# Kernel tuning notes

Measured on AMD Instinct MI355X. Metric: run time of the kernel, lower is better.

Reference implementation:

```python
import jax, jax.numpy as jnp
import numpy as np

EMB = 768
HEADS = 12
HD = EMB // HEADS
FF = 4 * EMB
EPS = 1e-5


def gelu_tanh(x):
    c = jnp.sqrt(jnp.asarray(2.0 / jnp.pi, x.dtype))
    return 0.5 * x * (1.0 + jnp.tanh(c * (x + 0.044715 * x ** 3)))


def layernorm(x, scale, shift):
    mean = x.mean(-1, keepdims=True)
    var = ((x - mean) ** 2).mean(-1, keepdims=True)
    return scale * (x - mean) / jnp.sqrt(var + EPS) + shift


def setup_inputs() -> dict:
    key = jax.random.key(0)
    ks = jax.random.split(key, 12)
    s = 0.02
    return {
        "x": jax.random.normal(ks[0], (8, 1024, EMB), jnp.float32),
        "Wq": jax.random.normal(ks[1], (EMB, EMB), jnp.float32) * s,
        "Wk": jax.random.normal(ks[2], (EMB, EMB), jnp.float32) * s,
        "Wv": jax.random.normal(ks[3], (EMB, EMB), jnp.float32) * s,
        "Wo": jax.random.normal(ks[4], (EMB, EMB), jnp.float32) * s,
        "bo": jnp.zeros((EMB,), jnp.float32),
        "W1": jax.random.normal(ks[5], (EMB, FF), jnp.float32) * s,
        "b1": jnp.zeros((FF,), jnp.float32),
        "W2": jax.random.normal(ks[6], (FF, EMB), jnp.float32) * s,
        "b2": jnp.zeros((EMB,), jnp.float32),
        "ln1_scale": jnp.ones((EMB,), jnp.float32),
        "ln1_shift": jnp.zeros((EMB,), jnp.float32),
        "ln2_scale": jnp.ones((EMB,), jnp.float32),
        "ln2_shift": jnp.zeros((EMB,), jnp.float32),
    }


def reference(x, Wq, Wk, Wv, Wo, bo, W1, b1, W2, b2,
              ln1_scale, ln1_shift, ln2_scale, ln2_shift):
    B, T, _ = x.shape
    inp = x
    h = layernorm(x, ln1_scale, ln1_shift)
    # QKV projections (no bias, qkv_bias=False)
    q = (h @ Wq).reshape(B, T, HEADS, HD).transpose(0, 2, 1, 3)  # [B,H,T,hd]
    k = (h @ Wk).reshape(B, T, HEADS, HD).transpose(0, 2, 1, 3)
    v = (h @ Wv).reshape(B, T, HEADS, HD).transpose(0, 2, 1, 3)
    scores = jnp.einsum('bhqd,bhkd->bhqk', q, k)
    causal = jnp.triu(jnp.ones((T, T), bool), k=1)
    scores = jnp.where(causal, -jnp.inf, scores)
    attn = jax.nn.softmax(scores / jnp.sqrt(jnp.asarray(HD, x.dtype)), axis=-1)
    ctx = jnp.einsum('bhqk,bhkd->bhqd', attn, v)
    ctx = ctx.transpose(0, 2, 1, 3).reshape(B, T, EMB)
    attn_out = ctx @ Wo + bo
    x = inp + attn_out  # dropout is identity (rate 0 / eval)
    inp = x
    h = layernorm(x, ln2_scale, ln2_shift)
    ff = gelu_tanh(h @ W1 + b1) @ W2 + b2
    return inp + ff
```

## Files before the change

### kernel.cpp

```cpp
#include <hip/hip_runtime.h>
#include <hip/hip_bf16.h>
#include <stdint.h>
#include <stddef.h>

#define EMB 768
#define FFD 3072
#define NHEAD 12
#define HD 64
#define SEQ 1024
#define NTOK 8192
#define QKVW 2304

typedef unsigned short u16;
typedef __attribute__((ext_vector_type(8))) short short8;
typedef __attribute__((ext_vector_type(4))) float f32x4;

__device__ __forceinline__ u16 f2bf(float f) {
  union { float f; uint32_t u; } w; w.f = f;
  uint32_t x = w.u + 0x7fffu + ((w.u >> 16) & 1u);
  return (u16)(x >> 16);
}

__device__ __forceinline__ uint32_t pkbf(float lo, float hi) {
  __hip_bfloat162 h = __float22bfloat162_rn(float2{lo, hi});
  union { __hip_bfloat162 h; uint32_t u; } cv; cv.h = h;
  return cv.u;
}

__device__ __forceinline__ void g2l16(const void* g, void* l) {
  __builtin_amdgcn_global_load_lds(
      (const __attribute__((address_space(1))) void*)g,
      (__attribute__((address_space(3))) void*)l, 16, 0, 0);
}

__global__ __launch_bounds__(256)
void transpose_kernel(const float* __restrict__ in, u16* __restrict__ out, int K, int N) {
  __shared__ float tile[32][33];
  const int n0 = blockIdx.x * 32, k0 = blockIdx.y * 32;
  const int tx = threadIdx.x & 31;
  const int ty = threadIdx.x >> 5;
#pragma unroll
  for (int i = 0; i < 32; i += 8)
    tile[ty + i][tx] = in[(size_t)(k0 + ty + i) * N + n0 + tx];
  __syncthreads();
#pragma unroll
  for (int i = 0; i < 32; i += 8)
    out[(size_t)(n0 + ty + i) * K + k0 + tx] = f2bf(tile[tx][ty + i]);
}

__global__ __launch_bounds__(256)
void transpose_qkv_kernel(const float* __restrict__ Wq, const float* __restrict__ Wk,
                          const float* __restrict__ Wv, u16* __restrict__ out) {
  __shared__ float tile[32][33];
  const float* in = blockIdx.z == 0 ? Wq : (blockIdx.z == 1 ? Wk : Wv);
  u16* o = out + (size_t)blockIdx.z * EMB * EMB;
  const int n0 = blockIdx.x * 32, k0 = blockIdx.y * 32;
  const int tx = threadIdx.x & 31;
  const int ty = threadIdx.x >> 5;
#pragma unroll
  for (int i = 0; i < 32; i += 8)
    tile[ty + i][tx] = in[(size_t)(k0 + ty + i) * EMB + n0 + tx];
  __syncthreads();
#pragma unroll
  for (int i = 0; i < 32; i += 8)
    o[(size_t)(n0 + ty + i) * EMB + k0 + tx] = f2bf(tile[tx][ty + i]);
}

__global__ __launch_bounds__(256)
void ln_kernel(const float* __restrict__ x, const float* __restrict__ sc,
               const float* __restrict__ sh, u16* __restrict__ out) {
  const int row = blockIdx.x;
  const int tid = threadIdx.x;
  const float* xr = x + (size_t)row * EMB;
  float v0 = xr[tid], v1 = xr[tid + 256], v2 = xr[tid + 512];
  float s = v0 + v1 + v2;
  float ss = v0 * v0 + v1 * v1 + v2 * v2;
#pragma unroll
  for (int m = 1; m < 64; m <<= 1) { s += __shfl_xor(s, m, 64); ss += __shfl_xor(ss, m, 64); }
  __shared__ float red[8];
  const int wave = tid >> 6, lane = tid & 63;
  if (lane == 0) { red[wave] = s; red[wave + 4] = ss; }
  __syncthreads();
  s = red[0] + red[1] + red[2] + red[3];
  ss = red[4] + red[5] + red[6] + red[7];
  const float mean = s * (1.f / EMB);
  const float var = ss * (1.f / EMB) - mean * mean;
  const float inv = rsqrtf(var + 1e-5f);
  u16* orow = out + (size_t)row * EMB;
  orow[tid]       = f2bf((v0 - mean) * inv * sc[tid]       + sh[tid]);
  orow[tid + 256] = f2bf((v1 - mean) * inv * sc[tid + 256] + sh[tid + 256]);
  orow[tid + 512] = f2bf((v2 - mean) * inv * sc[tid + 512] + sh[tid + 512]);
}

template <int EPI, int MT, bool SWAP>
__global__ __launch_bounds__(256)
void gemm_kernel(const u16* __restrict__ A, const u16* __restrict__ BT,
                 void* __restrict__ Cp, const float* __restrict__ bias,
                 const float* __restrict__ res, u16* __restrict__ vTp,
                 int M, int N, int K) {
  constexpr int MI = MT / 32;
  __shared__ u16 As[MT * 64];
  __shared__ u16 Bs[128 * 64];

  const int nwg = gridDim.x * gridDim.y;
  const int orig = blockIdx.y * gridDim.x + blockIdx.x;
  const int swz = (orig & 7) * (nwg >> 3) + (orig >> 3);
  const int m0 = (swz / gridDim.x) * MT;
  const int n0 = (swz % gridDim.x) * 128;

  const int tid = threadIdx.x;
  const int wave = tid >> 6, lane = tid & 63;
  const int wr = wave >> 1, wc = wave & 1;
  const int r = lane & 15, g = lane >> 4;
  const int lrow = lane >> 3;
  const int lelem = (lane & 7) * 8;

  f32x4 acc[MI][4] = {};

  const int nkt = K >> 6;
  for (int kt = 0; kt < nkt; ++kt) {
    const int k0 = kt << 6;
    if (kt) __syncthreads();
#pragma unroll
    for (int q = 0; q < MT / 32; ++q) {
      const int chunk = q * 4 + wave;
      const int row = chunk * 8 + lrow;
      const int e = lelem ^ ((row & 7) << 3);
      g2l16(A + (size_t)(m0 + row) * K + k0 + e, As + chunk * 512);
    }
#pragma unroll
    for (int q = 0; q < 4; ++q) {
      const int chunk = q * 4 + wave;
      const int row = chunk * 8 + lrow;
      const int e = lelem ^ ((row & 7) << 3);
      g2l16(BT + (size_t)(n0 + row) * K + k0 + e, Bs + chunk * 512);
    }
    __syncthreads();
#pragma unroll
    for (int kk = 0; kk < 2; ++kk) {
      short8 af[MI], bf[4];
#pragma unroll
      for (int mi = 0; mi < MI; ++mi) {
        const int row = wr * (MT / 2) + mi * 16 + r;
        af[mi] = *(const short8*)(As + row * 64 + ((kk * 32 + g * 8) ^ ((row & 7) << 3)));
      }
#pragma unroll
      for (int ni = 0; ni < 4; ++ni) {
        const int row = wc * 64 + ni * 16 + r;
        bf[ni] = *(const short8*)(Bs + row * 64 + ((kk * 32 + g * 8) ^ ((row & 7) << 3)));
      }
#pragma unroll
      for (int mi = 0; mi < MI; ++mi)
#pragma unroll
        for (int ni = 0; ni < 4; ++ni) {
          if constexpr (SWAP)
            acc[mi][ni] = __builtin_amdgcn_mfma_f32_16x16x32_bf16(bf[ni], af[mi], acc[mi][ni], 0, 0, 0);
          else
            acc[mi][ni] = __builtin_amdgcn_mfma_f32_16x16x32_bf16(af[mi], bf[ni], acc[mi][ni], 0, 0, 0);
        }
    }
  }

  if constexpr (SWAP) {
#pragma unroll
    for (int mi = 0; mi < MI; ++mi) {
      const int m = m0 + wr * (MT / 2) + mi * 16 + r;
#pragma unroll
      for (int ni = 0; ni < 4; ++ni) {
        const int nb = n0 + wc * 64 + ni * 16 + 4 * g;
        if constexpr (EPI == 1) {
          const float4 bs = *(const float4*)(bias + nb);
          const float4 rs = *(const float4*)(res + (size_t)m * N + nb);
          float4 o;
          o.x = acc[mi][ni][0] + bs.x + rs.x;
          o.y = acc[mi][ni][1] + bs.y + rs.y;
          o.z = acc[mi][ni][2] + bs.z + rs.z;
          o.w = acc[mi][ni][3] + bs.w + rs.w;
          *(float4*)((float*)Cp + (size_t)m * N + nb) = o;
        } else {
          const float4 bs = *(const float4*)(bias + nb);
          float tj[4];
#pragma unroll
          for (int j = 0; j < 4; ++j) {
            float t = acc[mi][ni][j] + (&bs.x)[j];
            float e = __expf(1.5957691216057308f * (t + 0.044715f * t * t * t));
            tj[j] = 0.5f * t * (1.f + (1.f - 2.f / (e + 1.f)));
          }
          uint2 w2;
          w2.x = pkbf(tj[0], tj[1]);
          w2.y = pkbf(tj[2], tj[3]);
          *(uint2*)((u16*)Cp + (size_t)m * N + nb) = w2;
        }
      }
    }
  } else {
#pragma unroll
    for (int mi = 0; mi < MI; ++mi)
#pragma unroll
      for (int ni = 0; ni < 4; ++ni) {
        const int rowb = m0 + wr * (MT / 2) + mi * 16 + 4 * g;
        const int col = n0 + wc * 64 + ni * 16 + r;
        u16 pk[4];
#pragma unroll
        for (int j = 0; j < 4; ++j) pk[j] = f2bf(acc[mi][ni][j]);
        if (col < 1536) {
#pragma unroll
          for (int j = 0; j < 4; ++j)
            ((u16*)Cp)[(size_t)(rowb + j) * N + col] = pk[j];
        } else {
          uint2 w2;
          w2.x = (uint32_t)pk[0] | ((uint32_t)pk[1] << 16);
          w2.y = (uint32_t)pk[2] | ((uint32_t)pk[3] << 16);
          *(uint2*)(vTp + (size_t)(col - 1536) * NTOK + rowb) = w2;
        }
      }
  }
}

#define CEXP 0.18033688011112042f

__global__ __launch_bounds__(256, 3)
void attn_kernel(const u16* __restrict__ qkv, const u16* __restrict__ vT,
                 u16* __restrict__ ctx) {
  const int bh = blockIdx.x;
  const int qt = blockIdx.y;
  const int b = bh / NHEAD, h = bh % NHEAD;
  const int tid = threadIdx.x;
  const int wave = tid >> 6, lane = tid & 63;
  const int r = lane & 15, g = lane >> 4;

  __shared__ u16 Kb[2][64 * 64];
  __shared__ u16 Vb[2][64 * 64];
  __shared__ u16 Pt[4][16 * 64];

  const int qw = qt * 128 + wave * 32;
  const int tok0 = b * SEQ;

  short8 aq[2][2];
#pragma unroll
  for (int qf = 0; qf < 2; ++qf) {
    const u16* qb = qkv + (size_t)(tok0 + qw + qf * 16 + r) * QKVW + h * HD;
    aq[qf][0] = *(const short8*)(qb + g * 8);
    aq[qf][1] = *(const short8*)(qb + 32 + g * 8);
  }

  float l_st[2] = {0.f, 0.f};
  f32x4 oc[2][4] = {};

  const int sr = tid >> 3;
  const int sc = (tid & 7) * 8;
  const int nt = 2 * qt + 2;

  const u16* kg = qkv + (size_t)tok0 * QKVW + EMB + h * HD;
  const u16* vg = vT + (size_t)(h * HD) * NTOK + tok0;
  const int e0 = sc ^ ((sr & 7) << 3);

  auto stage = [&](int buf, int kt) {
    const size_t koff = (size_t)kt * 64;
    u16* kb = (u16*)Kb[buf] + wave * 512;
    u16* vb = (u16*)Vb[buf] + wave * 512;
    g2l16(kg + (koff + sr) * QKVW + e0, kb);
    g2l16(kg + (koff + sr + 32) * QKVW + e0, kb + 2048);
    g2l16(vg + (size_t)sr * NTOK + koff + e0, vb);
    g2l16(vg + (size_t)(sr + 32) * NTOK + koff + e0, vb + 2048);
  };

  stage(0, 0);
  for (int kb = 0; kb < nt; ++kb) {
    __syncthreads();
    const int cur = kb & 1;
    if (kb + 1 < nt) stage(cur ^ 1, kb + 1);

    const int kv0 = kb * 64;
    if (kv0 > qw + 31) continue;

    short8 kf[4][2];
#pragma unroll
    for (int nf = 0; nf < 4; ++nf) {
      const int row = nf * 16 + r;
#pragma unroll
      for (int kk = 0; kk < 2; ++kk)
        kf[nf][kk] = *(const short8*)((char*)Kb[cur] + row * 128 +
                                      ((kk * 64 + g * 16) ^ ((row & 7) << 4)));
    }
    short8 bv[2][4];
#pragma unroll
    for (int half = 0; half < 2; ++half)
#pragma unroll
      for (int nd = 0; nd < 4; ++nd) {
        const int vr = nd * 16 + r;
        bv[half][nd] = *(const short8*)((char*)Vb[cur] + vr * 128 +
                       ((half * 64 + g * 16) ^ ((vr & 7) << 4)));
      }

#pragma unroll
    for (int qf = 0; qf < 2; ++qf) {
      f32x4 st[4];
#pragma unroll
      for (int nf = 0; nf < 4; ++nf) {
        f32x4 z = {};
        z = __builtin_amdgcn_mfma_f32_16x16x32_bf16(kf[nf][0], aq[qf][0], z, 0, 0, 0);
        z = __builtin_amdgcn_mfma_f32_16x16x32_bf16(kf[nf][1], aq[qf][1], z, 0, 0, 0);
        st[nf] = z;
      }
      if (kv0 + 63 > qw + qf * 16) {
        const int qg = qw + qf * 16 + r;
#pragma unroll
        for (int nf = 0; nf < 4; ++nf)
#pragma unroll
          for (int j = 0; j < 4; ++j)
            if (kv0 + nf * 16 + 4 * g + j > qg) st[nf][j] = -3e38f;
      }
      float p[4][4];
      float ps = 0.f;
#pragma unroll
      for (int nf = 0; nf < 4; ++nf)
#pragma unroll
        for (int j = 0; j < 4; ++j) {
          const float pe = exp2f(st[nf][j] * CEXP);
          p[nf][j] = pe;
          ps += pe;
        }
      ps += __shfl_xor(ps, 16);
      ps += __shfl_xor(ps, 32);
      l_st[qf] += ps;

      u16* Pw = (u16*)Pt[wave];
#pragma unroll
      for (int nf = 0; nf < 4; ++nf) {
        uint2 w2;
        w2.x = pkbf(p[nf][0], p[nf][1]);
        w2.y = pkbf(p[nf][2], p[nf][3]);
        *(uint2*)((char*)Pw + r * 128 + ((nf * 32 + g * 8) ^ ((r & 7) << 4))) = w2;
      }
#pragma unroll
      for (int half = 0; half < 2; ++half) {
        short8 pa = *(const short8*)((char*)Pw + r * 128 +
                                     ((half * 64 + g * 16) ^ ((r & 7) << 4)));
#pragma unroll
        for (int nd = 0; nd < 4; ++nd)
          oc[qf][nd] = __builtin_amdgcn_mfma_f32_16x16x32_bf16(pa, bv[half][nd], oc[qf][nd], 0, 0, 0);
      }
    }
  }

#pragma unroll
  for (int qf = 0; qf < 2; ++qf) {
    const float rl = 1.f / l_st[qf];
#pragma unroll
    for (int j = 0; j < 4; ++j) {
      const float rj = __shfl(rl, 4 * g + j, 16);
      const size_t row = (size_t)tok0 + qw + qf * 16 + 4 * g + j;
#pragma unroll
      for (int nd = 0; nd < 4; ++nd)
        ctx[row * EMB + h * HD + nd * 16 + r] = f2bf(oc[qf][nd][j] * rj);
    }
  }
}

extern "C" void kernel_launch(void* const* d_in, const int* in_sizes, int n_in,
                              void* d_out, int out_size, void* d_ws, size_t ws_size,
                              hipStream_t stream) {
  const float* x    = (const float*)d_in[0];
  const float* Wq   = (const float*)d_in[1];
  const float* Wk   = (const float*)d_in[2];
  const float* Wv   = (const float*)d_in[3];
  const float* Wo   = (const float*)d_in[4];
  const float* bo   = (const float*)d_in[5];
  const float* W1   = (const float*)d_in[6];
  const float* b1   = (const float*)d_in[7];
  const float* W2   = (const float*)d_in[8];
  const float* b2   = (const float*)d_in[9];
  const float* ln1s = (const float*)d_in[10];
  const float* ln1b = (const float*)d_in[11];
  const float* ln2s = (const float*)d_in[12];
  const float* ln2b = (const float*)d_in[13];

  char* p = (char*)d_ws;
  u16* qkvT = (u16*)p; p += (size_t)QKVW * EMB * 2;
  u16* woT  = (u16*)p; p += (size_t)EMB * EMB * 2;
  u16* w1T  = (u16*)p; p += (size_t)FFD * EMB * 2;
  u16* w2T  = (u16*)p; p += (size_t)EMB * FFD * 2;
  u16* h1   = (u16*)p; p += (size_t)NTOK * EMB * 2;
  u16* qkv  = (u16*)p; p += (size_t)NTOK * QKVW * 2;
  float* x2 = (float*)p; p += (size_t)NTOK * EMB * 4;
  u16* ff1  = (u16*)p; p += (size_t)NTOK * FFD * 2;
  u16* ctxb = h1;
  u16* h2   = qkv;
  u16* vT   = ff1;

  if (ws_size < (size_t)(p - (char*)d_ws)) return;

  dim3 blk(256);
  transpose_qkv_kernel<<<dim3(24, 24, 3), blk, 0, stream>>>(Wq, Wk, Wv, qkvT);
  transpose_kernel<<<dim3(24, 24), blk, 0, stream>>>(Wo, woT, EMB, EMB);
  transpose_kernel<<<dim3(96, 24), blk, 0, stream>>>(W1, w1T, EMB, FFD);
  transpose_kernel<<<dim3(24, 96), blk, 0, stream>>>(W2, w2T, FFD, EMB);

  ln_kernel<<<NTOK, blk, 0, stream>>>(x, ln1s, ln1b, h1);
  gemm_kernel<3, 128, false><<<dim3(18, 64), blk, 0, stream>>>(h1, qkvT, qkv, nullptr, nullptr, vT, NTOK, QKVW, EMB);
  attn_kernel<<<dim3(96, 8), blk, 0, stream>>>(qkv, vT, ctxb);
  gemm_kernel<1, 64, true><<<dim3(6, 128), blk, 0, stream>>>(ctxb, woT, x2, bo, x, nullptr, NTOK, EMB, EMB);
  ln_kernel<<<NTOK, blk, 0, stream>>>(x2, ln2s, ln2b, h2);
  gemm_kernel<2, 128, true><<<dim3(24, 64), blk, 0, stream>>>(h2, w1T, ff1, b1, nullptr, nullptr, NTOK, FFD, EMB);
  gemm_kernel<1, 64, true><<<dim3(6, 128), blk, 0, stream>>>(ff1, w2T, (float*)d_out, b2, x2, nullptr, NTOK, EMB, FFD);
}
```

Before: 233.6 us.

## Store residual in bf16, split QKV kernel with vectorized Q/K stores

Adds a dedicated QKV GEMM kernel that picks the MFMA operand order per tile, so the Q/K outputs use packed 64-bit row stores into a compact 1536-wide buffer instead of scattered 16-bit stores. V is still written transposed. The attention residual x2 is now stored in bf16 instead of fp32, with a new bf16 layernorm kernel and a bf16-residual epilogue in the final GEMM. This cuts write and read traffic, but rounding the residual stream to bf16 lowers accuracy.

```diff
diff --git a/kernel.cpp b/kernel.cpp
--- a/kernel.cpp
+++ b/kernel.cpp
@@ -10,6 +10,7 @@
 #define SEQ 1024
 #define NTOK 8192
 #define QKVW 2304
+#define QKW 1536
 
 typedef unsigned short u16;
 typedef __attribute__((ext_vector_type(8))) short short8;
@@ -19,6 +20,10 @@
   union { float f; uint32_t u; } w; w.f = f;
   uint32_t x = w.u + 0x7fffu + ((w.u >> 16) & 1u);
   return (u16)(x >> 16);
+}
+
+__device__ __forceinline__ float bf2f(uint32_t v) {
+  union { uint32_t u; float f; } c; c.u = v << 16; return c.f;
 }
 
 __device__ __forceinline__ uint32_t pkbf(float lo, float hi) {
@@ -92,11 +97,37 @@
   orow[tid + 512] = f2bf((v2 - mean) * inv * sc[tid + 512] + sh[tid + 512]);
 }
 
+__global__ __launch_bounds__(256)
+void ln_bf_kernel(const u16* __restrict__ x, const float* __restrict__ sc,
+                  const float* __restrict__ sh, u16* __restrict__ out) {
+  const int row = blockIdx.x;
+  const int tid = threadIdx.x;
+  const u16* xr = x + (size_t)row * EMB;
+  float v0 = bf2f(xr[tid]), v1 = bf2f(xr[tid + 256]), v2 = bf2f(xr[tid + 512]);
+  float s = v0 + v1 + v2;
+  float ss = v0 * v0 + v1 * v1 + v2 * v2;
+#pragma unroll
+  for (int m = 1; m < 64; m <<= 1) { s += __shfl_xor(s, m, 64); ss += __shfl_xor(ss, m, 64); }
+  __shared__ float red[8];
+  const int wave = tid >> 6, lane = tid & 63;
+  if (lane == 0) { red[wave] = s; red[wave + 4] = ss; }
+  __syncthreads();
+  s = red[0] + red[1] + red[2] + red[3];
+  ss = red[4] + red[5] + red[6] + red[7];
+  const float mean = s * (1.f / EMB);
+  const float var = ss * (1.f / EMB) - mean * mean;
+  const float inv = rsqrtf(var + 1e-5f);
+  u16* orow = out + (size_t)row * EMB;
+  orow[tid]       = f2bf((v0 - mean) * inv * sc[tid]       + sh[tid]);
+  orow[tid + 256] = f2bf((v1 - mean) * inv * sc[tid + 256] + sh[tid + 256]);
+  orow[tid + 512] = f2bf((v2 - mean) * inv * sc[tid + 512] + sh[tid + 512]);
+}
+
 template <int EPI, int MT, bool SWAP>
 __global__ __launch_bounds__(256)
 void gemm_kernel(const u16* __restrict__ A, const u16* __restrict__ BT,
                  void* __restrict__ Cp, const float* __restrict__ bias,
-                 const float* __restrict__ res, u16* __restrict__ vTp,
+                 const float* __restrict__ res, const u16* __restrict__ res16,
                  int M, int N, int K) {
   constexpr int MI = MT / 32;
   __shared__ u16 As[MT * 64];
@@ -161,36 +192,137 @@
     }
   }
 
-  if constexpr (SWAP) {
+#pragma unroll
+  for (int mi = 0; mi < MI; ++mi) {
+    const int m = m0 + wr * (MT / 2) + mi * 16 + r;
+#pragma unroll
+    for (int ni = 0; ni < 4; ++ni) {
+      const int nb = n0 + wc * 64 + ni * 16 + 4 * g;
+      if constexpr (EPI == 1) {
+        const float4 bs = *(const float4*)(bias + nb);
+        const float4 rs = *(const float4*)(res + (size_t)m * N + nb);
+        float4 o;
+        o.x = acc[mi][ni][0] + bs.x + rs.x;
+        o.y = acc[mi][ni][1] + bs.y + rs.y;
+        o.z = acc[mi][ni][2] + bs.z + rs.z;
+        o.w = acc[mi][ni][3] + bs.w + rs.w;
+        *(float4*)((float*)Cp + (size_t)m * N + nb) = o;
+      } else if constexpr (EPI == 2) {
+        const float4 bs = *(const float4*)(bias + nb);
+        float tj[4];
+#pragma unroll
+        for (int j = 0; j < 4; ++j) {
+          float t = acc[mi][ni][j] + (&bs.x)[j];
+          float e = __expf(1.5957691216057308f * (t + 0.044715f * t * t * t));
+          tj[j] = 0.5f * t * (1.f + (1.f - 2.f / (e + 1.f)));
+        }
+        uint2 w2;
+        w2.x = pkbf(tj[0], tj[1]);
+        w2.y = pkbf(tj[2], tj[3]);
+        *(uint2*)((u16*)Cp + (size_t)m * N + nb) = w2;
+      } else if constexpr (EPI == 4) {
+        const float4 bs = *(const float4*)(bias + nb);
+        const float4 rs = *(const float4*)(res + (size_t)m * N + nb);
+        uint2 w2;
+        w2.x = pkbf(acc[mi][ni][0] + bs.x + rs.x, acc[mi][ni][1] + bs.y + rs.y);
+        w2.y = pkbf(acc[mi][ni][2] + bs.z + rs.z, acc[mi][ni][3] + bs.w + rs.w);
+        *(uint2*)((u16*)Cp + (size_t)m * N + nb) = w2;
+      } else {
+        const float4 bs = *(const float4*)(bias + nb);
+        const uint2 r2 = *(const uint2*)(res16 + (size_t)m * N + nb);
+        float4 o;
+        o.x = acc[mi][ni][0] + bs.x + bf2f(r2.x & 0xffffu);
+        o.y = acc[mi][ni][1] + bs.y + bf2f(r2.x >> 16);
+        o.z = acc[mi][ni][2] + bs.z + bf2f(r2.y & 0xffffu);
+        o.w = acc[mi][ni][3] + bs.w + bf2f(r2.y >> 16);
+        *(float4*)((float*)Cp + (size_t)m * N + nb) = o;
+      }
+    }
+  }
+}
+
+__global__ __launch_bounds__(256)
+void qkv_kernel(const u16* __restrict__ A, const u16* __restrict__ BT,
+                u16* __restrict__ qkp, u16* __restrict__ vTp) {
+  constexpr int MT = 128, MI = 4, K = EMB, N = QKVW;
+  __shared__ u16 As[MT * 64];
+  __shared__ u16 Bs[128 * 64];
+
+  const int nwg = gridDim.x * gridDim.y;
+  const int orig = blockIdx.y * gridDim.x + blockIdx.x;
+  const int swz = (orig & 7) * (nwg >> 3) + (orig >> 3);
+  const int m0 = (swz / gridDim.x) * MT;
+  const int n0 = (swz % gridDim.x) * 128;
+
+  const int tid = threadIdx.x;
+  const int wave = tid >> 6, lane = tid & 63;
+  const int wr = wave >> 1, wc = wave & 1;
+  const int r = lane & 15, g = lane >> 4;
+  const int lrow = lane >> 3;
+  const int lelem = (lane & 7) * 8;
+
+  f32x4 acc[MI][4] = {};
+  const bool isQK = (n0 < 1536);
+
+  const int nkt = K >> 6;
+  for (int kt = 0; kt < nkt; ++kt) {
+    const int k0 = kt << 6;
+    if (kt) __syncthreads();
+#pragma unroll
+    for (int q = 0; q < MT / 32; ++q) {
+      const int chunk = q * 4 + wave;
+      const int row = chunk * 8 + lrow;
+      const int e = lelem ^ ((row & 7) << 3);
+      g2l16(A + (size_t)(m0 + row) * K + k0 + e, As + chunk * 512);
+    }
+#pragma unroll
+    for (int q = 0; q < 4; ++q) {
+      const int chunk = q * 4 + wave;
+      const int row = chunk * 8 + lrow;
+      const int e = lelem ^ ((row & 7) << 3);
+      g2l16(BT + (size_t)(n0 + row) * K + k0 + e, Bs + chunk * 512);
+    }
+    __syncthreads();
+#pragma unroll
+    for (int kk = 0; kk < 2; ++kk) {
+      short8 af[MI], bf[4];
+#pragma unroll
+      for (int mi = 0; mi < MI; ++mi) {
+        const int row = wr * (MT / 2) + mi * 16 + r;
+        af[mi] = *(const short8*)(As + row * 64 + ((kk * 32 + g * 8) ^ ((row & 7) << 3)));
+      }
+#pragma unroll
+      for (int ni = 0; ni < 4; ++ni) {
+        const int row = wc * 64 + ni * 16 + r;
+        bf[ni] = *(const short8*)(Bs + row * 64 + ((kk * 32 + g * 8) ^ ((row & 7) << 3)));
+      }
+      if (isQK) {
+#pragma unroll
+        for (int mi = 0; mi < MI; ++mi)
+#pragma unroll
+          for (int ni = 0; ni < 4; ++ni)
+            acc[mi][ni] = __builtin_amdgcn_mfma_f32_16x16x32_bf16(bf[ni], af[mi], acc[mi][ni], 0, 0, 0);
+      } else {
+#pragma unroll
+        for (int mi = 0; mi < MI; ++mi)
+#pragma unroll
+          for (int ni = 0; ni < 4; ++ni)
+            acc[mi][ni] = __builtin_amdgcn_mfma_f32_16x16x32_bf16(af[mi], bf[ni], acc[mi][ni], 0, 0, 0);
+      }
+    }
+  }
+
+  if (isQK) {
 #pragma unroll
     for (int mi = 0; mi < MI; ++mi) {
       const int m = m0 + wr * (MT / 2) + mi * 16 + r;
 #pragma unroll
       for (int ni = 0; ni < 4; ++ni) {
         const int nb = n0 + wc * 64 + ni * 16 + 4 * g;
-        if constexpr (EPI == 1) {
-          const float4 bs = *(const float4*)(bias + nb);
-          const float4 rs = *(const float4*)(res + (size_t)m * N + nb);
-          float4 o;
-          o.x = acc[mi][ni][0] + bs.x + rs.x;
-          o.y = acc[mi][ni][1] + bs.y + rs.y;
-          o.z = acc[mi][ni][2] + bs.z + rs.z;
-          o.w = acc[mi][ni][3] + bs.w + rs.w;
-          *(float4*)((float*)Cp + (size_t)m * N + nb) = o;
-        } else {
-          const float4 bs = *(const float4*)(bias + nb);
-          float tj[4];
-#pragma unroll
-          for (int j = 0; j < 4; ++j) {
-            float t = acc[mi][ni][j] + (&bs.x)[j];
-            float e = __expf(1.5957691216057308f * (t + 0.044715f * t * t * t));
-            tj[j] = 0.5f * t * (1.f + (1.f - 2.f / (e + 1.f)));
-          }
-          uint2 w2;
-          w2.x = pkbf(tj[0], tj[1]);
-          w2.y = pkbf(tj[2], tj[3]);
-          *(uint2*)((u16*)Cp + (size_t)m * N + nb) = w2;
-        }
+        uint2 w2;
+        w2.x = pkbf(acc[mi][ni][0], acc[mi][ni][1]);
+        w2.y = pkbf(acc[mi][ni][2], acc[mi][ni][3]);
+        *(uint2*)(qkp + (size_t)m * QKW + nb) = w2;
       }
     }
   } else {
@@ -200,19 +332,10 @@
       for (int ni = 0; ni < 4; ++ni) {
         const int rowb = m0 + wr * (MT / 2) + mi * 16 + 4 * g;
         const int col = n0 + wc * 64 + ni * 16 + r;
-        u16 pk[4];
-#pragma unroll
-        for (int j = 0; j < 4; ++j) pk[j] = f2bf(acc[mi][ni][j]);
-        if (col < 1536) {
-#pragma unroll
-          for (int j = 0; j < 4; ++j)
-            ((u16*)Cp)[(size_t)(rowb + j) * N + col] = pk[j];
-        } else {
-          uint2 w2;
-          w2.x = (uint32_t)pk[0] | ((uint32_t)pk[1] << 16);
-          w2.y = (uint32_t)pk[2] | ((uint32_t)pk[3] << 16);
-          *(uint2*)(vTp + (size_t)(col - 1536) * NTOK + rowb) = w2;
-        }
+        uint2 w2;
+        w2.x = pkbf(acc[mi][ni][0], acc[mi][ni][1]);
+        w2.y = pkbf(acc[mi][ni][2], acc[mi][ni][3]);
+        *(uint2*)(vTp + (size_t)(col - 1536) * NTOK + rowb) = w2;
       }
   }
 }
@@ -220,7 +343,7 @@
 #define CEXP 0.18033688011112042f
 
 __global__ __launch_bounds__(256, 3)
-void attn_kernel(const u16* __restrict__ qkv, const u16* __restrict__ vT,
+void attn_kernel(const u16* __restrict__ qk, const u16* __restrict__ vT,
                  u16* __restrict__ ctx) {
   const int bh = blockIdx.x;
   const int qt = blockIdx.y;
@@ -239,7 +362,7 @@
   short8 aq[2][2];
 #pragma unroll
   for (int qf = 0; qf < 2; ++qf) {
-    const u16* qb = qkv + (size_t)(tok0 + qw + qf * 16 + r) * QKVW + h * HD;
+    const u16* qb = qk + (size_t)(tok0 + qw + qf * 16 + r) * QKW + h * HD;
     aq[qf][0] = *(const short8*)(qb + g * 8);
     aq[qf][1] = *(const short8*)(qb + 32 + g * 8);
   }
@@ -251,7 +374,7 @@
   const int sc = (tid & 7) * 8;
   const int nt = 2 * qt + 2;
 
-  const u16* kg = qkv + (size_t)tok0 * QKVW + EMB + h * HD;
+  const u16* kg = qk + (size_t)tok0 * QKW + EMB + h * HD;
   const u16* vg = vT + (size_t)(h * HD) * NTOK + tok0;
   const int e0 = sc ^ ((sr & 7) << 3);
 
@@ -259,8 +382,8 @@
     const size_t koff = (size_t)kt * 64;
     u16* kb = (u16*)Kb[buf] + wave * 512;
     u16* vb = (u16*)Vb[buf] + wave * 512;
-    g2l16(kg + (koff + sr) * QKVW + e0, kb);
-    g2l16(kg + (koff + sr + 32) * QKVW + e0, kb + 2048);
+    g2l16(kg + (koff + sr) * QKW + e0, kb);
+    g2l16(kg + (koff + sr + 32) * QKW + e0, kb + 2048);
     g2l16(vg + (size_t)sr * NTOK + koff + e0, vb);
     g2l16(vg + (size_t)(sr + 32) * NTOK + koff + e0, vb + 2048);
   };
@@ -382,11 +505,11 @@
   u16* w1T  = (u16*)p; p += (size_t)FFD * EMB * 2;
   u16* w2T  = (u16*)p; p += (size_t)EMB * FFD * 2;
   u16* h1   = (u16*)p; p += (size_t)NTOK * EMB * 2;
-  u16* qkv  = (u16*)p; p += (size_t)NTOK * QKVW * 2;
-  float* x2 = (float*)p; p += (size_t)NTOK * EMB * 4;
+  u16* qk   = (u16*)p; p += (size_t)NTOK * QKW * 2;
+  u16* x2bf = (u16*)p; p += (size_t)NTOK * EMB * 2;
   u16* ff1  = (u16*)p; p += (size_t)NTOK * FFD * 2;
   u16* ctxb = h1;
-  u16* h2   = qkv;
+  u16* h2   = qk;
   u16* vT   = ff1;
 
   if (ws_size < (size_t)(p - (char*)d_ws)) return;
@@ -398,10 +521,10 @@
   transpose_kernel<<<dim3(24, 96), blk, 0, stream>>>(W2, w2T, FFD, EMB);
 
   ln_kernel<<<NTOK, blk, 0, stream>>>(x, ln1s, ln1b, h1);
-  gemm_kernel<3, 128, false><<<dim3(18, 64), blk, 0, stream>>>(h1, qkvT, qkv, nullptr, nullptr, vT, NTOK, QKVW, EMB);
-  attn_kernel<<<dim3(96, 8), blk, 0, stream>>>(qkv, vT, ctxb);
-  gemm_kernel<1, 64, true><<<dim3(6, 128), blk, 0, stream>>>(ctxb, woT, x2, bo, x, nullptr, NTOK, EMB, EMB);
-  ln_kernel<<<NTOK, blk, 0, stream>>>(x2, ln2s, ln2b, h2);
+  qkv_kernel<<<dim3(18, 64), blk, 0, stream>>>(h1, qkvT, qk, vT);
+  attn_kernel<<<dim3(96, 8), blk, 0, stream>>>(qk, vT, ctxb);
+  gemm_kernel<4, 64, true><<<dim3(6, 128), blk, 0, stream>>>(ctxb, woT, x2bf, bo, x, nullptr, NTOK, EMB, EMB);
+  ln_bf_kernel<<<NTOK, blk, 0, stream>>>(x2bf, ln2s, ln2b, h2);
   gemm_kernel<2, 128, true><<<dim3(24, 64), blk, 0, stream>>>(h2, w1T, ff1, b1, nullptr, nullptr, NTOK, FFD, EMB);
-  gemm_kernel<1, 64, true><<<dim3(6, 128), blk, 0, stream>>>(ff1, w2T, (float*)d_out, b2, x2, nullptr, NTOK, EMB, FFD);
-}
+  gemm_kernel<5, 64, true><<<dim3(6, 128), blk, 0, stream>>>(ff1, w2T, (float*)d_out, b2, nullptr, x2bf, NTOK, EMB, FFD);
+}
```

Result: slower. 245.4 us (+5.1%).
